# Performance work log

Measured on AMD Instinct MI355X. Metric: run time of the kernel, lower is better.

The kernel has to match this reference:

```python
import jax, jax.numpy as jnp
import numpy as np

D_MODEL = 2048
NUM_HEADS = 16
D_HEAD = D_MODEL // NUM_HEADS
ROPE_THETA = 10000.0
MAX_SEQ_LEN = 2048
NEG_INF = -1e30


def _rope_tables(seq_len):
    pos = jnp.arange(seq_len, dtype=jnp.float32)[:, None]          # [s,1]
    i = jnp.arange(0, D_HEAD, 2, dtype=jnp.float32)                 # [d/2]
    freqs = 1.0 / (ROPE_THETA ** (i / D_HEAD))
    angles = pos * freqs                                            # [s, d/2]
    return jnp.cos(angles), jnp.sin(angles)


def _apply_rope(x, cos, sin):
    # x: [b,h,s,d]; interleaved pairs: x1 = even dims, x2 = odd dims
    x1 = x[..., 0::2]
    x2 = x[..., 1::2]
    r1 = x1 * cos - x2 * sin
    r2 = x1 * sin + x2 * cos
    return jnp.stack([r1, r2], axis=-1).reshape(x.shape)


def setup_inputs() -> dict:
    key = jax.random.key(0)
    ks = jax.random.split(key, 5)
    b, s = 2, 2048
    scale = 1.0 / np.sqrt(D_MODEL)  # ~kaiming fan_in scale
    return {
        "x": jax.random.normal(ks[0], (b, s, D_MODEL), jnp.float32),
        "Wq": jax.random.normal(ks[1], (D_MODEL, D_MODEL), jnp.float32) * scale,
        "bq": jnp.zeros((D_MODEL,), jnp.float32),
        "Wk": jax.random.normal(ks[2], (D_MODEL, D_MODEL), jnp.float32) * scale,
        "bk": jnp.zeros((D_MODEL,), jnp.float32),
        "Wv": jax.random.normal(ks[3], (D_MODEL, D_MODEL), jnp.float32) * scale,
        "bv": jnp.zeros((D_MODEL,), jnp.float32),
        "Wo": jax.random.normal(ks[4], (D_MODEL, D_MODEL), jnp.float32) * scale,
        "bo": jnp.zeros((D_MODEL,), jnp.float32),
    }


def reference(x, Wq, bq, Wk, bk, Wv, bv, Wo, bo):
    b, s, _ = x.shape
    # QKV projections (torch Linear: y = x @ W.T + b)
    q = x @ Wq.T + bq
    k = x @ Wk.T + bk
    v = x @ Wv.T + bv
    # split heads: b s (h d) -> b h s d
    def split(t):
        return t.reshape(b, s, NUM_HEADS, D_HEAD).transpose(0, 2, 1, 3)
    q, k, v = split(q), split(k), split(v)
    # RoPE
    cos, sin = _rope_tables(s)
    q = _apply_rope(q, cos, sin)
    k = _apply_rope(k, cos, sin)
    # scaled dot-product attention with causal mask
    scores = jnp.einsum('bhqd,bhkd->bhqk', q, k) / jnp.sqrt(jnp.float32(D_HEAD))
    causal = jnp.tril(jnp.ones((s, s), dtype=bool))
    scores = jnp.where(causal[None, None], scores, NEG_INF)
    attn = jax.nn.softmax(scores, axis=-1)
    out = jnp.einsum('bhqk,bhkd->bhqd', attn, v)
    # merge heads and output projection
    out = out.transpose(0, 2, 1, 3).reshape(b, s, D_MODEL)
    return out @ Wo.T + bo
```

## Files before the change

### kernel.cpp

```cpp
#include <hip/hip_runtime.h>
#include <hip/hip_fp16.h>
#include <math.h>

#define D_MODEL 2048
#define NH 16
#define DH 128
#define SEQ 2048
#define NBH 32

typedef unsigned short u16;
typedef unsigned int u32;
typedef __attribute__((ext_vector_type(8))) short short8;
typedef __attribute__((ext_vector_type(4))) float floatx4;
typedef __attribute__((ext_vector_type(2))) unsigned int uint2v;
typedef __attribute__((ext_vector_type(4))) unsigned int uint4v;
typedef __attribute__((ext_vector_type(4))) unsigned short ushort4v;

__device__ __forceinline__ u16 f2bf(float f) {
  u32 u = __builtin_bit_cast(u32, f);
  return (u16)((u + 0x8000u) >> 16);
}
__device__ __forceinline__ float bf2f(u16 h) {
  return __builtin_bit_cast(float, (u32)h << 16);
}

__device__ __forceinline__ void async_load16(const u16* g, u16* l) {
  __builtin_amdgcn_global_load_lds(
      (const __attribute__((address_space(1))) void*)g,
      (__attribute__((address_space(3))) void*)l, 16, 0, 0);
}

__global__ void cvt_kernel(const float* __restrict__ src, u16* __restrict__ dst,
                           int n) {
  const int i = (blockIdx.x * 256 + threadIdx.x) * 8;
  if (i >= n) return;
  const floatx4 a = *(const floatx4*)(src + i);
  const floatx4 b = *(const floatx4*)(src + i + 4);
  short8 h;
  h[0] = (short)f2bf(a[0]); h[1] = (short)f2bf(a[1]);
  h[2] = (short)f2bf(a[2]); h[3] = (short)f2bf(a[3]);
  h[4] = (short)f2bf(b[0]); h[5] = (short)f2bf(b[1]);
  h[6] = (short)f2bf(b[2]); h[7] = (short)f2bf(b[3]);
  *(short8*)(dst + i) = h;
}

__global__ void cvt4_kernel(const float* __restrict__ x,
                            const float* __restrict__ wq,
                            const float* __restrict__ wk,
                            const float* __restrict__ wv, u16* __restrict__ xb,
                            u16* __restrict__ wqb, u16* __restrict__ wkb,
                            u16* __restrict__ wvb, u32* __restrict__ rtab) {
  const int blk = blockIdx.x;
  if (blk >= 10240) {
    const int e0 = ((blk - 10240) * 256 + threadIdx.x) * 4;
#pragma unroll
    for (int e = e0; e < e0 + 4; ++e) {
      const int s = e >> 6, p = e & 63;
      const float freq = exp2f(-(float)p * (13.287712379549449f / 64.0f));
      float sn, cs;
      sincosf((float)s * freq, &sn, &cs);
      rtab[e] = (u32)__half_as_ushort(__float2half_rn(cs)) |
                ((u32)__half_as_ushort(__float2half_rn(sn)) << 16);
    }
    return;
  }
  const float* src;
  u16* dst;
  int base;
  if (blk < 4096) {
    src = x; dst = xb; base = blk;
  } else if (blk < 6144) {
    src = wq; dst = wqb; base = blk - 4096;
  } else if (blk < 8192) {
    src = wk; dst = wkb; base = blk - 6144;
  } else {
    src = wv; dst = wvb; base = blk - 8192;
  }
  const int i = (base * 256 + threadIdx.x) * 8;
  const floatx4 a = *(const floatx4*)(src + i);
  const floatx4 b = *(const floatx4*)(src + i + 4);
  short8 h;
  h[0] = (short)f2bf(a[0]); h[1] = (short)f2bf(a[1]);
  h[2] = (short)f2bf(a[2]); h[3] = (short)f2bf(a[3]);
  h[4] = (short)f2bf(b[0]); h[5] = (short)f2bf(b[1]);
  h[6] = (short)f2bf(b[2]); h[7] = (short)f2bf(b[3]);
  *(short8*)(dst + i) = h;
}

__global__ __launch_bounds__(256, 2) void gemm_async(
    const u16* __restrict__ A, const u16* __restrict__ W0,
    const u16* __restrict__ W1, const u16* __restrict__ W2,
    const float* __restrict__ b0, const float* __restrict__ b1,
    const float* __restrict__ b2, void* __restrict__ C0, void* __restrict__ C1,
    void* __restrict__ C2, const u32* __restrict__ rtab, const int qkv) {
  __shared__ u16 smem[2 * 128 * 64];
  u16* const As = smem;
  u16* const Bs = smem + 128 * 64;
  const int tid = threadIdx.x;
  const int wave = tid >> 6, lane = tid & 63;
  const int lr = lane & 15, lg = lane >> 4;
  const int m0 = blockIdx.y * 128;
  const int wm = (wave & 1) * 64, wn = (wave >> 1) * 64;

  int n0, mode;
  const u16* W;
  const float* bias;
  void* C;
  if (qkv) {
    const int which = blockIdx.x >> 4;
    n0 = (blockIdx.x & 15) * 128;
    W = which == 0 ? W0 : which == 1 ? W1 : W2;
    bias = which == 0 ? b0 : which == 1 ? b1 : b2;
    C = which == 0 ? C0 : which == 1 ? C1 : C2;
    mode = which;
  } else {
    n0 = blockIdx.x * 128;
    W = W0; bias = b0; C = C0; mode = 3;
  }

  floatx4 acc[4][4];
#pragma unroll
  for (int i = 0; i < 4; ++i)
#pragma unroll
    for (int j = 0; j < 4; ++j) {
      floatx4 z = {0.f, 0.f, 0.f, 0.f};
      acc[i][j] = z;
    }

  for (int kt = 0; kt < D_MODEL; kt += 64) {
#pragma unroll
    for (int p = 0; p < 4; ++p) {
      const int s = p * 256 + tid;
      const int row = s >> 3, c = s & 7;
      const int g = c ^ (row & 7);
      async_load16(A + (size_t)(m0 + row) * D_MODEL + kt + g * 8,
                   &As[(p * 256 + wave * 64) * 8]);
    }
#pragma unroll
    for (int p = 0; p < 4; ++p) {
      const int s = p * 256 + tid;
      const int row = s >> 3, c = s & 7;
      const int g = c ^ (row & 7);
      async_load16(W + (size_t)(n0 + row) * D_MODEL + kt + g * 8,
                   &Bs[(p * 256 + wave * 64) * 8]);
    }
    __syncthreads();

#pragma unroll
    for (int ks = 0; ks < 2; ++ks) {
      short8 af[4], bfr[4];
      const int ch = (ks * 4 + lg) ^ (lr & 7);
#pragma unroll
      for (int i = 0; i < 4; ++i)
        af[i] = *(const short8*)&As[(wm + 16 * i + lr) * 64 + ch * 8];
#pragma unroll
      for (int j = 0; j < 4; ++j)
        bfr[j] = *(const short8*)&Bs[(wn + 16 * j + lr) * 64 + ch * 8];
#pragma unroll
      for (int i = 0; i < 4; ++i)
#pragma unroll
        for (int j = 0; j < 4; ++j)
          acc[i][j] = __builtin_amdgcn_mfma_f32_16x16x32_bf16(af[i], bfr[j],
                                                              acc[i][j], 0, 0, 0);
    }
    __syncthreads();
  }

  float bj[4];
  int ncol[4];
#pragma unroll
  for (int j = 0; j < 4; ++j) {
    ncol[j] = n0 + wn + 16 * j + lr;
    bj[j] = bias[ncol[j]];
  }

  if (mode == 3) {
    float* Cf = (float*)C;
#pragma unroll
    for (int i = 0; i < 4; ++i)
#pragma unroll
      for (int r = 0; r < 4; ++r) {
        const int m = m0 + wm + 16 * i + lg * 4 + r;
#pragma unroll
        for (int j = 0; j < 4; ++j)
          Cf[(size_t)m * D_MODEL + ncol[j]] = acc[i][j][r] + bj[j];
      }
  } else if (mode == 2) {
    u16* Ch = (u16*)C;
#pragma unroll
    for (int i = 0; i < 4; ++i)
#pragma unroll
      for (int r = 0; r < 4; ++r) {
        const int m = m0 + wm + 16 * i + lg * 4 + r;
        const int b = m >> 11, s = m & (SEQ - 1);
#pragma unroll
        for (int j = 0; j < 4; ++j) {
          const int h = ncol[j] >> 7, d = ncol[j] & (DH - 1);
          Ch[((size_t)((b * NH + h) * DH + d)) * SEQ + s] =
              f2bf(acc[i][j][r] + bj[j]);
        }
      }
  } else {
    u32* tab = (u32*)smem;
    {
      const u32* slice = rtab + (size_t)(m0 & (SEQ - 1)) * 64;
#pragma unroll
      for (int kk = 0; kk < 8; ++kk)
        ((uint4v*)tab)[kk * 256 + tid] = ((const uint4v*)slice)[kk * 256 + tid];
    }
    __syncthreads();
    u16* Ch = (u16*)C;
    int pj[4];
#pragma unroll
    for (int j = 0; j < 4; ++j) pj[j] = (ncol[j] & (DH - 1)) >> 1;
    const bool odd = (lr & 1) != 0;
#pragma unroll
    for (int i = 0; i < 4; ++i)
#pragma unroll
      for (int r = 0; r < 4; ++r) {
        const int mloc = wm + 16 * i + lg * 4 + r;
        const int m = m0 + mloc;
        const int b = m >> 11, s = m & (SEQ - 1);
#pragma unroll
        for (int j = 0; j < 4; ++j) {
          const float val = acc[i][j][r] + bj[j];
          const float partner = __shfl_xor(val, 1);
          const u32 cw = tab[mloc * 64 + pj[j]];
          const float cs = __half2float(__ushort_as_half((u16)(cw & 0xffffu)));
          const float sn = __half2float(__ushort_as_half((u16)(cw >> 16)));
          const float outv = odd ? fmaf(partner, sn, val * cs)
                                 : fmaf(partner, -sn, val * cs);
          const int h = ncol[j] >> 7, d = ncol[j] & (DH - 1);
          Ch[((size_t)((b * NH + h) * SEQ + s)) * DH + d] = f2bf(outv);
        }
      }
  }
}

__global__ void rope_kernel(u16* __restrict__ Q, u16* __restrict__ K) {
  const int idx = blockIdx.x * blockDim.x + threadIdx.x;
  const int p = idx & 63;
  const int s = (idx >> 6) & (SEQ - 1);
  const int bh = idx >> 17;
  if (bh >= NBH) return;
  const float freq = exp2f(-(float)p * (13.287712379549449f / 64.0f));
  const float ang = (float)s * freq;
  float sn, cs;
  sincosf(ang, &sn, &cs);
  const size_t base = ((size_t)bh * SEQ + s) * DH + 2 * p;
  {
    const u32 qq = *(const u32*)(Q + base);
    const float x1 = bf2f((u16)(qq & 0xffffu)), x2 = bf2f((u16)(qq >> 16));
    *(u32*)(Q + base) =
        (u32)f2bf(x1 * cs - x2 * sn) | ((u32)f2bf(x1 * sn + x2 * cs) << 16);
  }
  {
    const u32 kk = *(const u32*)(K + base);
    const float x1 = bf2f((u16)(kk & 0xffffu)), x2 = bf2f((u16)(kk >> 16));
    *(u32*)(K + base) =
        (u32)f2bf(x1 * cs - x2 * sn) | ((u32)f2bf(x1 * sn + x2 * cs) << 16);
  }
}

__global__ __launch_bounds__(256, 2) void attn_kernel(
    const u16* __restrict__ Q, const u16* __restrict__ K,
    const u16* __restrict__ Vt, u16* __restrict__ Oflat) {
  __shared__ u16 Ks[2][64 * 128];
  __shared__ u16 Vts[128 * 64];
  __shared__ u16 Ps[4 * 32 * 72];
  const int tid = threadIdx.x;
  const int wave = tid >> 6, lane = tid & 63;
  const int lr = lane & 15, lg = lane >> 4;
  const int L = blockIdx.y * 16 + blockIdx.x;
  const int bh = L & 31;
  const int t = L >> 5;
  const int qt = (t < 8) ? t : 23 - t;
  const size_t qk0 = (size_t)bh * SEQ * DH;
  const int q0 = qt * 128 + wave * 32;
  const float C = 0.12752602f;
  const float RTHR = 62.7f;

  short8 qf[2][4];
#pragma unroll
  for (int i = 0; i < 2; ++i)
#pragma unroll
    for (int kb = 0; kb < 4; ++kb)
      qf[i][kb] = *(const short8*)(Q + qk0 + (size_t)(q0 + 16 * i + lr) * DH +
                                   kb * 32 + lg * 8);

  floatx4 o[2][9];
#pragma unroll
  for (int i = 0; i < 2; ++i)
#pragma unroll
    for (int jd = 0; jd < 9; ++jd) {
      floatx4 z = {0.f, 0.f, 0.f, 0.f};
      o[i][jd] = z;
    }
  float mrun[2] = {-1e38f, -1e38f};

  const short8 onesv = {16256, 16256, 16256, 16256,
                        16256, 16256, 16256, 16256};

  u16* myP = &Ps[wave * 32 * 72];
  const int nkt = 2 * qt + 2;

#pragma unroll
  for (int p = 0; p < 4; ++p) {
    const int s = p * 256 + tid;
    const int row = s >> 4, c = s & 15;
    const int g = c ^ (row & 15);
    async_load16(K + qk0 + (size_t)row * DH + g * 8,
                 &Ks[0][(p * 256 + wave * 64) * 8]);
  }
  __syncthreads();

  for (int kt = 0; kt < nkt; ++kt) {
    const int cur = kt & 1, nb = cur ^ 1;
    const int kn = (kt + 1 < nkt) ? kt + 1 : kt;
#pragma unroll
    for (int p = 0; p < 4; ++p) {
      const int s = p * 256 + tid;
      const int row = s >> 3, c = s & 7;
      const int g = c ^ (row & 7);
      async_load16(Vt + (size_t)bh * DH * SEQ + (size_t)row * SEQ + kt * 64 + g * 8,
                   &Vts[(p * 256 + wave * 64) * 8]);
    }
#pragma unroll
    for (int p = 0; p < 4; ++p) {
      const int s = p * 256 + tid;
      const int row = s >> 4, c = s & 15;
      const int g = c ^ (row & 15);
      async_load16(K + qk0 + (size_t)(kn * 64 + row) * DH + g * 8,
                   &Ks[nb][(p * 256 + wave * 64) * 8]);
    }

    floatx4 st[4][2];
#pragma unroll
    for (int j = 0; j < 4; ++j)
#pragma unroll
      for (int i = 0; i < 2; ++i) {
        floatx4 z = {0.f, 0.f, 0.f, 0.f};
        st[j][i] = z;
      }
#pragma unroll
    for (int kb = 0; kb < 4; ++kb) {
      short8 kf[4];
#pragma unroll
      for (int j = 0; j < 4; ++j)
        kf[j] = *(const short8*)&Ks[cur][(16 * j + lr) * 128 +
                                         (((kb * 4 + lg) ^ lr)) * 8];
      __builtin_amdgcn_s_setprio(1);
#pragma unroll
      for (int j = 0; j < 4; ++j)
#pragma unroll
        for (int i = 0; i < 2; ++i)
          st[j][i] = __builtin_amdgcn_mfma_f32_16x16x32_bf16(kf[j], qf[i][kb],
                                                             st[j][i], 0, 0, 0);
      __builtin_amdgcn_s_setprio(0);
    }

    if (kt >= 2 * qt) {
#pragma unroll
      for (int j = 0; j < 4; ++j)
#pragma unroll
        for (int i = 0; i < 2; ++i)
#pragma unroll
          for (int r = 0; r < 4; ++r) {
            const int kpos = kt * 64 + 16 * j + 4 * lg + r;
            const int qpos = q0 + 16 * i + lr;
            if (kpos > qpos) st[j][i][r] = -1e30f;
          }
    }

    float mx[2];
#pragma unroll
    for (int i = 0; i < 2; ++i) {
      float m0v = fmaxf(fmaxf(st[0][i][0], st[0][i][1]),
                        fmaxf(st[0][i][2], st[0][i][3]));
      float m1v = fmaxf(fmaxf(st[1][i][0], st[1][i][1]),
                        fmaxf(st[1][i][2], st[1][i][3]));
      float m2v = fmaxf(fmaxf(st[2][i][0], st[2][i][1]),
                        fmaxf(st[2][i][2], st[2][i][3]));
      float m3v = fmaxf(fmaxf(st[3][i][0], st[3][i][1]),
                        fmaxf(st[3][i][2], st[3][i][3]));
      float m = fmaxf(fmaxf(m0v, m1v), fmaxf(m2v, m3v));
      m = fmaxf(m, __shfl_xor(m, 16));
      m = fmaxf(m, __shfl_xor(m, 32));
      mx[i] = m;
    }
    const float grow = fmaxf(mx[0] - mrun[0], mx[1] - mrun[1]);
    if (!__all(grow <= RTHR)) {
      float aS[2];
#pragma unroll
      for (int i = 0; i < 2; ++i) {
        const float mn = fmaxf(mrun[i], mx[i]);
        aS[i] = exp2f((mrun[i] - mn) * C);
        mrun[i] = mn;
      }
#pragma unroll
      for (int i = 0; i < 2; ++i)
#pragma unroll
        for (int r = 0; r < 4; ++r) {
          const float aO = __shfl(aS[i], 4 * lg + r);
#pragma unroll
          for (int jd = 0; jd < 9; ++jd) o[i][jd][r] *= aO;
        }
    }
    float negMC[2];
#pragma unroll
    for (int i = 0; i < 2; ++i) negMC[i] = -mrun[i] * C;

#pragma unroll
    for (int i = 0; i < 2; ++i)
#pragma unroll
      for (int j = 0; j < 4; ++j) {
        const float p0 = exp2f(fmaf(st[j][i][0], C, negMC[i]));
        const float p1 = exp2f(fmaf(st[j][i][1], C, negMC[i]));
        const float p2 = exp2f(fmaf(st[j][i][2], C, negMC[i]));
        const float p3 = exp2f(fmaf(st[j][i][3], C, negMC[i]));
        uint2v w;
        w[0] = (u32)f2bf(p0) | ((u32)f2bf(p1) << 16);
        w[1] = (u32)f2bf(p2) | ((u32)f2bf(p3) << 16);
        *(uint2v*)&myP[(16 * i + lr) * 72 + 16 * j + 4 * lg] = w;
      }

    asm volatile("s_waitcnt lgkmcnt(0)" ::: "memory");
    __syncthreads();

#pragma unroll
    for (int kb = 0; kb < 2; ++kb) {
      short8 pf[2];
#pragma unroll
      for (int i = 0; i < 2; ++i)
        pf[i] = *(const short8*)&myP[(16 * i + lr) * 72 + kb * 32 + lg * 8];
      __builtin_amdgcn_s_setprio(1);
#pragma unroll
      for (int jd = 0; jd < 8; ++jd) {
        const short8 vf = *(const short8*)&Vts[(16 * jd + lr) * 64 +
                                               (((kb * 4 + lg) ^ (lr & 7))) * 8];
#pragma unroll
        for (int i = 0; i < 2; ++i)
          o[i][jd] = __builtin_amdgcn_mfma_f32_16x16x32_bf16(pf[i], vf, o[i][jd],
                                                             0, 0, 0);
      }
#pragma unroll
      for (int i = 0; i < 2; ++i)
        o[i][8] = __builtin_amdgcn_mfma_f32_16x16x32_bf16(pf[i], onesv, o[i][8],
                                                          0, 0, 0);
      __builtin_amdgcn_s_setprio(0);
    }
    __syncthreads();
  }

  const int b = bh >> 4, h = bh & (NH - 1);
#pragma unroll
  for (int i = 0; i < 2; ++i)
#pragma unroll
    for (int r = 0; r < 4; ++r) {
      const int qpos = q0 + 16 * i + lg * 4 + r;
      const float inv = 1.0f / o[i][8][r];
      u16* dst = Oflat + ((size_t)(b * SEQ + qpos)) * D_MODEL + h * DH;
#pragma unroll
      for (int jd = 0; jd < 8; ++jd) dst[16 * jd + lr] = f2bf(o[i][jd][r] * inv);
    }
}

template <int ABF16>
__global__ __launch_bounds__(256, 2) void gemm_kernel(
    const void* __restrict__ Aptr, const float* __restrict__ W,
    const float* __restrict__ bias, void* __restrict__ Cptr, const int mode) {
  __shared__ u16 As[128 * 72];
  __shared__ u16 Bs[128 * 72];
  const int tid = threadIdx.x;
  const int wave = tid >> 6, lane = tid & 63;
  const int lr = lane & 15, lg = lane >> 4;
  const int m0 = blockIdx.y * 128, n0 = blockIdx.x * 128;
  const int wm = (wave & 1) * 64, wn = (wave >> 1) * 64;

  floatx4 acc[4][4];
#pragma unroll
  for (int i = 0; i < 4; ++i)
#pragma unroll
    for (int j = 0; j < 4; ++j) {
      floatx4 z = {0.f, 0.f, 0.f, 0.f};
      acc[i][j] = z;
    }

  for (int kt = 0; kt < D_MODEL; kt += 64) {
    if (ABF16) {
      const u16* A = (const u16*)Aptr;
      const int row0 = tid >> 3, c8 = (tid & 7) * 8;
#pragma unroll
      for (int p = 0; p < 4; ++p) {
        const int row = row0 + p * 32;
        *(short8*)&As[row * 72 + c8] =
            *(const short8*)(A + (size_t)(m0 + row) * D_MODEL + kt + c8);
      }
    } else {
      const float* A = (const float*)Aptr;
      const int row0 = tid >> 4, c4 = (tid & 15) * 4;
#pragma unroll
      for (int p = 0; p < 8; ++p) {
        const int row = row0 + p * 16;
        const floatx4 v =
            *(const floatx4*)(A + (size_t)(m0 + row) * D_MODEL + kt + c4);
        ushort4v h;
        h[0] = f2bf(v[0]); h[1] = f2bf(v[1]); h[2] = f2bf(v[2]); h[3] = f2bf(v[3]);
        *(ushort4v*)&As[row * 72 + c4] = h;
      }
    }
    {
      const int row0 = tid >> 4, c4 = (tid & 15) * 4;
#pragma unroll
      for (int p = 0; p < 8; ++p) {
        const int row = row0 + p * 16;
        const floatx4 v =
            *(const floatx4*)(W + (size_t)(n0 + row) * D_MODEL + kt + c4);
        ushort4v h;
        h[0] = f2bf(v[0]); h[1] = f2bf(v[1]); h[2] = f2bf(v[2]); h[3] = f2bf(v[3]);
        *(ushort4v*)&Bs[row * 72 + c4] = h;
      }
    }
    __syncthreads();
#pragma unroll
    for (int ks = 0; ks < 2; ++ks) {
      short8 af[4], bfr[4];
#pragma unroll
      for (int i = 0; i < 4; ++i)
        af[i] = *(const short8*)&As[(wm + 16 * i + lr) * 72 + ks * 32 + lg * 8];
#pragma unroll
      for (int j = 0; j < 4; ++j)
        bfr[j] = *(const short8*)&Bs[(wn + 16 * j + lr) * 72 + ks * 32 + lg * 8];
#pragma unroll
      for (int i = 0; i < 4; ++i)
#pragma unroll
        for (int j = 0; j < 4; ++j)
          acc[i][j] = __builtin_amdgcn_mfma_f32_16x16x32_bf16(af[i], bfr[j],
                                                              acc[i][j], 0, 0, 0);
    }
    __syncthreads();
  }

  float bj[4];
  int ncol[4];
#pragma unroll
  for (int j = 0; j < 4; ++j) {
    ncol[j] = n0 + wn + 16 * j + lr;
    bj[j] = bias[ncol[j]];
  }

  if (mode == 3) {
    float* C = (float*)Cptr;
#pragma unroll
    for (int i = 0; i < 4; ++i)
#pragma unroll
      for (int r = 0; r < 4; ++r) {
        const int m = m0 + wm + 16 * i + lg * 4 + r;
#pragma unroll
        for (int j = 0; j < 4; ++j)
          C[(size_t)m * D_MODEL + ncol[j]] = acc[i][j][r] + bj[j];
      }
  } else if (mode == 2) {
    u16* C = (u16*)Cptr;
#pragma unroll
    for (int i = 0; i < 4; ++i)
#pragma unroll
      for (int r = 0; r < 4; ++r) {
        const int m = m0 + wm + 16 * i + lg * 4 + r;
        const int b = m >> 11, s = m & (SEQ - 1);
#pragma unroll
        for (int j = 0; j < 4; ++j) {
          const int h = ncol[j] >> 7, d = ncol[j] & (DH - 1);
          C[((size_t)((b * NH + h) * DH + d)) * SEQ + s] = f2bf(acc[i][j][r] + bj[j]);
        }
      }
  } else {
    u16* C = (u16*)Cptr;
#pragma unroll
    for (int i = 0; i < 4; ++i)
#pragma unroll
      for (int r = 0; r < 4; ++r) {
        const int m = m0 + wm + 16 * i + lg * 4 + r;
        const int b = m >> 11, s = m & (SEQ - 1);
#pragma unroll
        for (int j = 0; j < 4; ++j) {
          const int h = ncol[j] >> 7, d = ncol[j] & (DH - 1);
          C[((size_t)((b * NH + h) * SEQ + s)) * DH + d] = f2bf(acc[i][j][r] + bj[j]);
        }
      }
  }
}

extern "C" void kernel_launch(void* const* d_in, const int* in_sizes, int n_in,
                              void* d_out, int out_size, void* d_ws,
                              size_t ws_size, hipStream_t stream) {
  const float* x = (const float*)d_in[0];
  const float* Wq = (const float*)d_in[1];
  const float* bq = (const float*)d_in[2];
  const float* Wk = (const float*)d_in[3];
  const float* bk = (const float*)d_in[4];
  const float* Wv = (const float*)d_in[5];
  const float* bv = (const float*)d_in[6];
  const float* Wo = (const float*)d_in[7];
  const float* bo = (const float*)d_in[8];
  float* out = (float*)d_out;

  const size_t E = (size_t)NBH * SEQ * DH;
  const size_t WE = (size_t)D_MODEL * D_MODEL;
  const size_t need = (4 * E + 3 * WE) * sizeof(u16);

  const dim3 gb(256);

  if (ws_size >= need) {
    u16* xb = (u16*)d_ws;
    u16* wqb = xb + E;
    u16* wkb = wqb + WE;
    u16* wvb = wkb + WE;
    u16* q = wvb + WE;
    u16* k = q + E;
    u16* vt = k + E;
    u16* aflat = xb;
    u16* wob = q;
    u32* rtab = (u32*)out;

    cvt4_kernel<<<dim3(10368), gb, 0, stream>>>(x, Wq, Wk, Wv, xb, wqb, wkb,
                                                wvb, rtab);

    gemm_async<<<dim3(48, 32), gb, 0, stream>>>(xb, wqb, wkb, wvb, bq, bk, bv,
                                                q, k, vt, rtab, 1);
    attn_kernel<<<dim3(SEQ / 128, NBH), gb, 0, stream>>>(q, k, vt, aflat);
    cvt_kernel<<<dim3((int)(WE / 2048)), gb, 0, stream>>>(Wo, wob, (int)WE);
    gemm_async<<<dim3(16, 32), gb, 0, stream>>>(aflat, wob, nullptr, nullptr,
                                                bo, nullptr, nullptr, out,
                                                nullptr, nullptr, nullptr, 0);
  } else {
    u16* q = (u16*)d_ws;
    u16* k = q + E;
    u16* vt = k + E;
    u16* aflat = vt + E;
    const dim3 gg(D_MODEL / 128, (2 * SEQ) / 128);
    gemm_kernel<0><<<gg, gb, 0, stream>>>(x, Wq, bq, q, 0);
    gemm_kernel<0><<<gg, gb, 0, stream>>>(x, Wk, bk, k, 1);
    gemm_kernel<0><<<gg, gb, 0, stream>>>(x, Wv, bv, vt, 2);
    rope_kernel<<<dim3((NBH * SEQ * (DH / 2)) / 256), dim3(256), 0, stream>>>(q, k);
    attn_kernel<<<dim3(SEQ / 128, NBH), gb, 0, stream>>>(q, k, vt, aflat);
    gemm_kernel<1><<<gg, gb, 0, stream>>>(aflat, Wo, bo, out, 3);
  }
}
```

Baseline: 377.5 us.

## Add 256x256-tile QKV GEMM kernel with 512 threads and XCD-aware block remap

Replaces the 128x128-tile QKV projection GEMM with a new kernel that computes 256x256 output tiles using 8 waves and double-buffered async LDS staging. It interleaves the next-tile loads with the MFMA phases and remaps block IDs so neighbouring tiles land on the same XCD. The larger tile raises arithmetic intensity and cuts global and L2 traffic per FLOP. In exchange the grid has only 384 blocks at one block per CU, which risks under-filling the 256 CUs in the last wave, and the fused RoPE/bias epilogue needs a larger register footprint.

```diff
diff --git a/kernel.cpp b/kernel.cpp
--- a/kernel.cpp
+++ b/kernel.cpp
@@ -85,6 +85,173 @@
   h[4] = (short)f2bf(b[0]); h[5] = (short)f2bf(b[1]);
   h[6] = (short)f2bf(b[2]); h[7] = (short)f2bf(b[3]);
   *(short8*)(dst + i) = h;
+}
+
+__global__ __launch_bounds__(512, 1) void gemm256(
+    const u16* __restrict__ A, const u16* __restrict__ W0,
+    const u16* __restrict__ W1, const u16* __restrict__ W2,
+    const float* __restrict__ b0, const float* __restrict__ b1,
+    const float* __restrict__ b2, u16* __restrict__ C0, u16* __restrict__ C1,
+    u16* __restrict__ C2, const u32* __restrict__ rtab) {
+  __shared__ u16 lds[2][2][16384];
+  const int tid = threadIdx.x;
+  const int wid = tid >> 6, lane = tid & 63;
+  const int lr = lane & 15, lg = lane >> 4;
+  const int wm2 = wid >> 2, wn2 = wid & 3;
+
+  const int L = blockIdx.y * 24 + blockIdx.x;
+  const int wg = (L & 7) * 48 + (L >> 3);
+  const int bx = wg % 24, by = wg / 24;
+  const int which = bx >> 3;
+  const int n0 = (bx & 7) * 256;
+  const int m0 = by * 256;
+  const u16* W = which == 0 ? W0 : which == 1 ? W1 : W2;
+  const float* bias = which == 0 ? b0 : which == 1 ? b1 : b2;
+  u16* Ch = which == 0 ? C0 : which == 1 ? C1 : C2;
+
+  auto stage_half = [&](u16* dst, const u16* src, int rowBase, int ktOff) {
+#pragma unroll
+    for (int l = 0; l < 2; ++l) {
+      const int s2 = l * 512 + tid;
+      const int row = s2 >> 3, c = s2 & 7;
+      const int g = c ^ (row & 7);
+      async_load16(src + (size_t)(rowBase + row) * D_MODEL + ktOff + g * 8,
+                   dst + (l * 512 + wid * 64) * 8);
+    }
+  };
+
+  floatx4 acc[8][4];
+#pragma unroll
+  for (int i = 0; i < 8; ++i)
+#pragma unroll
+    for (int j = 0; j < 4; ++j) {
+      floatx4 z = {0.f, 0.f, 0.f, 0.f};
+      acc[i][j] = z;
+    }
+
+  stage_half(&lds[0][0][0],    A, m0,       0);
+  stage_half(&lds[0][0][8192], A, m0 + 128, 0);
+  stage_half(&lds[0][1][0],    W, n0,       0);
+  stage_half(&lds[0][1][8192], W, n0 + 128, 0);
+  __builtin_amdgcn_sched_barrier(0);
+  asm volatile("s_waitcnt vmcnt(0)" ::: "memory");
+  __builtin_amdgcn_sched_barrier(0);
+  __builtin_amdgcn_s_barrier();
+
+  for (int u = 0; u < 32; ++u) {
+    const int cb = u & 1, nb = cb ^ 1;
+    const u16* Ab = &lds[cb][0][0];
+    const u16* Bb = &lds[cb][1][0];
+    u16* An = &lds[nb][0][0];
+    u16* Bn = &lds[nb][1][0];
+    const int kn = (u + 1) * 64;
+    const bool pf = (u + 1 < 32);
+    short8 bfr[4][2];
+#pragma unroll
+    for (int p = 0; p < 4; ++p) {
+      if (p == 0) {
+#pragma unroll
+        for (int j = 0; j < 4; ++j) {
+          const int col = wn2 * 64 + 16 * j + lr;
+#pragma unroll
+          for (int ks = 0; ks < 2; ++ks)
+            bfr[j][ks] =
+                *(const short8*)&Bb[col * 64 + (((ks * 4 + lg) ^ (col & 7))) * 8];
+        }
+      }
+      short8 af[2][2];
+#pragma unroll
+      for (int ii = 0; ii < 2; ++ii) {
+        const int row = wm2 * 128 + 16 * (2 * p + ii) + lr;
+#pragma unroll
+        for (int ks = 0; ks < 2; ++ks)
+          af[ii][ks] =
+              *(const short8*)&Ab[row * 64 + (((ks * 4 + lg) ^ (row & 7))) * 8];
+      }
+      if (pf && p == 0) {
+        stage_half(An,        A, m0,       kn);
+        stage_half(An + 8192, A, m0 + 128, kn);
+      }
+      if (pf && p == 1) {
+        stage_half(Bn,        W, n0,       kn);
+        stage_half(Bn + 8192, W, n0 + 128, kn);
+      }
+      __builtin_amdgcn_sched_barrier(0);
+      __builtin_amdgcn_s_barrier();
+      asm volatile("s_waitcnt lgkmcnt(0)" ::: "memory");
+      __builtin_amdgcn_sched_barrier(0);
+      __builtin_amdgcn_s_setprio(1);
+#pragma unroll
+      for (int ks = 0; ks < 2; ++ks)
+#pragma unroll
+        for (int ii = 0; ii < 2; ++ii)
+#pragma unroll
+          for (int j = 0; j < 4; ++j)
+            acc[2 * p + ii][j] = __builtin_amdgcn_mfma_f32_16x16x32_bf16(
+                af[ii][ks], bfr[j][ks], acc[2 * p + ii][j], 0, 0, 0);
+      __builtin_amdgcn_s_setprio(0);
+      __builtin_amdgcn_sched_barrier(0);
+      if (p == 3 && pf) {
+        asm volatile("s_waitcnt vmcnt(0)" ::: "memory");
+        __builtin_amdgcn_sched_barrier(0);
+      }
+      __builtin_amdgcn_s_barrier();
+    }
+  }
+
+  float bj[4];
+  int ncol[4], pj[4];
+#pragma unroll
+  for (int j = 0; j < 4; ++j) {
+    ncol[j] = n0 + wn2 * 64 + 16 * j + lr;
+    bj[j] = bias[ncol[j]];
+    pj[j] = (ncol[j] & (DH - 1)) >> 1;
+  }
+
+  if (which < 2) {
+    u32* tab = (u32*)&lds[0][0][0];
+    const u32* slice = rtab + (size_t)(m0 & (SEQ - 1)) * 64;
+#pragma unroll
+    for (int kk = 0; kk < 8; ++kk)
+      ((uint4v*)tab)[kk * 512 + tid] = ((const uint4v*)slice)[kk * 512 + tid];
+    __syncthreads();
+    const bool odd = (lr & 1) != 0;
+#pragma unroll
+    for (int i = 0; i < 8; ++i)
+#pragma unroll
+      for (int r = 0; r < 4; ++r) {
+        const int row = wm2 * 128 + 16 * i + 4 * lg + r;
+        const int m = m0 + row;
+        const int b = m >> 11, s = m & (SEQ - 1);
+#pragma unroll
+        for (int j = 0; j < 4; ++j) {
+          const float val = acc[i][j][r] + bj[j];
+          const float partner = __shfl_xor(val, 1);
+          const u32 cw = tab[row * 64 + pj[j]];
+          const float cs = __half2float(__ushort_as_half((u16)(cw & 0xffffu)));
+          const float sn = __half2float(__ushort_as_half((u16)(cw >> 16)));
+          const float outv = odd ? fmaf(partner, sn, val * cs)
+                                 : fmaf(partner, -sn, val * cs);
+          const int h = ncol[j] >> 7, d = ncol[j] & (DH - 1);
+          Ch[((size_t)((b * NH + h) * SEQ + s)) * DH + d] = f2bf(outv);
+        }
+      }
+  } else {
+#pragma unroll
+    for (int i = 0; i < 8; ++i)
+#pragma unroll
+      for (int r = 0; r < 4; ++r) {
+        const int row = wm2 * 128 + 16 * i + 4 * lg + r;
+        const int m = m0 + row;
+        const int b = m >> 11, s = m & (SEQ - 1);
+#pragma unroll
+        for (int j = 0; j < 4; ++j) {
+          const int h = ncol[j] >> 7, d = ncol[j] & (DH - 1);
+          Ch[((size_t)((b * NH + h) * DH + d)) * SEQ + s] =
+              f2bf(acc[i][j][r] + bj[j]);
+        }
+      }
+  }
 }
 
 __global__ __launch_bounds__(256, 2) void gemm_async(
@@ -626,8 +793,8 @@
     cvt4_kernel<<<dim3(10368), gb, 0, stream>>>(x, Wq, Wk, Wv, xb, wqb, wkb,
                                                 wvb, rtab);
 
-    gemm_async<<<dim3(48, 32), gb, 0, stream>>>(xb, wqb, wkb, wvb, bq, bk, bv,
-                                                q, k, vt, rtab, 1);
+    gemm256<<<dim3(24, 16), dim3(512), 0, stream>>>(xb, wqb, wkb, wvb, bq, bk,
+                                                    bv, q, k, vt, rtab);
     attn_kernel<<<dim3(SEQ / 128, NBH), gb, 0, stream>>>(q, k, vt, aflat);
     cvt_kernel<<<dim3((int)(WE / 2048)), gb, 0, stream>>>(Wo, wob, (int)WE);
     gemm_async<<<dim3(16, 32), gb, 0, stream>>>(aflat, wob, nullptr, nullptr,
```

Measured after the change: 383.9 us. About the same (+1.7%).

## Load V fragments directly to registers in attention and fold Wo conversion into cvt4

Applied to the files above, without the earlier changes.

The attention kernel stops staging the transposed V tile through shared memory. Each lane now loads its V MFMA fragments straight from global memory into registers, in two halves placed around the QK^T compute, and one block-wide barrier per iteration is removed. Separately, when the workspace is large enough, the Wo fp32-to-bf16 conversion is merged into the first conversion kernel, which drops one kernel launch. The trade is more register pressure and uncoalesced global reads of V, which rely on L2 reuse, in exchange for less LDS traffic and fewer synchronisations.

```diff
diff --git a/kernel.cpp b/kernel.cpp
--- a/kernel.cpp
+++ b/kernel.cpp
@@ -47,12 +47,14 @@
 __global__ void cvt4_kernel(const float* __restrict__ x,
                             const float* __restrict__ wq,
                             const float* __restrict__ wk,
-                            const float* __restrict__ wv, u16* __restrict__ xb,
+                            const float* __restrict__ wv,
+                            const float* __restrict__ w3, u16* __restrict__ xb,
                             u16* __restrict__ wqb, u16* __restrict__ wkb,
-                            u16* __restrict__ wvb, u32* __restrict__ rtab) {
+                            u16* __restrict__ wvb, u16* __restrict__ w3b,
+                            u32* __restrict__ rtab, const int nconv) {
   const int blk = blockIdx.x;
-  if (blk >= 10240) {
-    const int e0 = ((blk - 10240) * 256 + threadIdx.x) * 4;
+  if (blk >= nconv) {
+    const int e0 = ((blk - nconv) * 256 + threadIdx.x) * 4;
 #pragma unroll
     for (int e = e0; e < e0 + 4; ++e) {
       const int s = e >> 6, p = e & 63;
@@ -73,8 +75,10 @@
     src = wq; dst = wqb; base = blk - 4096;
   } else if (blk < 8192) {
     src = wk; dst = wkb; base = blk - 6144;
+  } else if (blk < 10240) {
+    src = wv; dst = wvb; base = blk - 8192;
   } else {
-    src = wv; dst = wvb; base = blk - 8192;
+    src = w3; dst = w3b; base = blk - 10240;
   }
   const int i = (base * 256 + threadIdx.x) * 8;
   const floatx4 a = *(const floatx4*)(src + i);
@@ -266,7 +270,6 @@
     const u16* __restrict__ Q, const u16* __restrict__ K,
     const u16* __restrict__ Vt, u16* __restrict__ Oflat) {
   __shared__ u16 Ks[2][64 * 128];
-  __shared__ u16 Vts[128 * 64];
   __shared__ u16 Ps[4 * 32 * 72];
   const int tid = threadIdx.x;
   const int wave = tid >> 6, lane = tid & 63;
@@ -303,6 +306,7 @@
 
   u16* myP = &Ps[wave * 32 * 72];
   const int nkt = 2 * qt + 2;
+  const u16* vb = Vt + (size_t)bh * DH * SEQ;
 
 #pragma unroll
   for (int p = 0; p < 4; ++p) {
@@ -317,14 +321,12 @@
   for (int kt = 0; kt < nkt; ++kt) {
     const int cur = kt & 1, nb = cur ^ 1;
     const int kn = (kt + 1 < nkt) ? kt + 1 : kt;
-#pragma unroll
-    for (int p = 0; p < 4; ++p) {
-      const int s = p * 256 + tid;
-      const int row = s >> 3, c = s & 7;
-      const int g = c ^ (row & 7);
-      async_load16(Vt + (size_t)bh * DH * SEQ + (size_t)row * SEQ + kt * 64 + g * 8,
-                   &Vts[(p * 256 + wave * 64) * 8]);
-    }
+
+    short8 v0[8];
+#pragma unroll
+    for (int jd = 0; jd < 8; ++jd)
+      v0[jd] = *(const short8*)(vb + (size_t)(16 * jd + lr) * SEQ + kt * 64 +
+                                lg * 8);
 #pragma unroll
     for (int p = 0; p < 4; ++p) {
       const int s = p * 256 + tid;
@@ -358,6 +360,12 @@
                                                              st[j][i], 0, 0, 0);
       __builtin_amdgcn_s_setprio(0);
     }
+
+    short8 v1[8];
+#pragma unroll
+    for (int jd = 0; jd < 8; ++jd)
+      v1[jd] = *(const short8*)(vb + (size_t)(16 * jd + lr) * SEQ + kt * 64 +
+                                32 + lg * 8);
 
     if (kt >= 2 * qt) {
 #pragma unroll
@@ -425,7 +433,6 @@
       }
 
     asm volatile("s_waitcnt lgkmcnt(0)" ::: "memory");
-    __syncthreads();
 
 #pragma unroll
     for (int kb = 0; kb < 2; ++kb) {
@@ -436,8 +443,7 @@
       __builtin_amdgcn_s_setprio(1);
 #pragma unroll
       for (int jd = 0; jd < 8; ++jd) {
-        const short8 vf = *(const short8*)&Vts[(16 * jd + lr) * 64 +
-                                               (((kb * 4 + lg) ^ (lr & 7))) * 8];
+        const short8 vf = (kb == 0) ? v0[jd] : v1[jd];
 #pragma unroll
         for (int i = 0; i < 2; ++i)
           o[i][jd] = __builtin_amdgcn_mfma_f32_16x16x32_bf16(pf[i], vf, o[i][jd],
@@ -608,6 +614,7 @@
   const size_t E = (size_t)NBH * SEQ * DH;
   const size_t WE = (size_t)D_MODEL * D_MODEL;
   const size_t need = (4 * E + 3 * WE) * sizeof(u16);
+  const size_t need2 = (4 * E + 4 * WE) * sizeof(u16);
 
   const dim3 gb(256);
 
@@ -620,19 +627,31 @@
     u16* k = q + E;
     u16* vt = k + E;
     u16* aflat = xb;
-    u16* wob = q;
     u32* rtab = (u32*)out;
 
-    cvt4_kernel<<<dim3(10368), gb, 0, stream>>>(x, Wq, Wk, Wv, xb, wqb, wkb,
-                                                wvb, rtab);
-
-    gemm_async<<<dim3(48, 32), gb, 0, stream>>>(xb, wqb, wkb, wvb, bq, bk, bv,
-                                                q, k, vt, rtab, 1);
-    attn_kernel<<<dim3(SEQ / 128, NBH), gb, 0, stream>>>(q, k, vt, aflat);
-    cvt_kernel<<<dim3((int)(WE / 2048)), gb, 0, stream>>>(Wo, wob, (int)WE);
-    gemm_async<<<dim3(16, 32), gb, 0, stream>>>(aflat, wob, nullptr, nullptr,
-                                                bo, nullptr, nullptr, out,
-                                                nullptr, nullptr, nullptr, 0);
+    if (ws_size >= need2) {
+      u16* wob = vt + E;
+      cvt4_kernel<<<dim3(12416), gb, 0, stream>>>(x, Wq, Wk, Wv, Wo, xb, wqb,
+                                                  wkb, wvb, wob, rtab, 12288);
+      gemm_async<<<dim3(48, 32), gb, 0, stream>>>(xb, wqb, wkb, wvb, bq, bk,
+                                                  bv, q, k, vt, rtab, 1);
+      attn_kernel<<<dim3(SEQ / 128, NBH), gb, 0, stream>>>(q, k, vt, aflat);
+      gemm_async<<<dim3(16, 32), gb, 0, stream>>>(aflat, wob, nullptr, nullptr,
+                                                  bo, nullptr, nullptr, out,
+                                                  nullptr, nullptr, nullptr, 0);
+    } else {
+      u16* wob = q;
+      cvt4_kernel<<<dim3(10368), gb, 0, stream>>>(x, Wq, Wk, Wv, nullptr, xb,
+                                                  wqb, wkb, wvb, nullptr, rtab,
+                                                  10240);
+      gemm_async<<<dim3(48, 32), gb, 0, stream>>>(xb, wqb, wkb, wvb, bq, bk,
+                                                  bv, q, k, vt, rtab, 1);
+      attn_kernel<<<dim3(SEQ / 128, NBH), gb, 0, stream>>>(q, k, vt, aflat);
+      cvt_kernel<<<dim3((int)(WE / 2048)), gb, 0, stream>>>(Wo, wob, (int)WE);
+      gemm_async<<<dim3(16, 32), gb, 0, stream>>>(aflat, wob, nullptr, nullptr,
+                                                  bo, nullptr, nullptr, out,
+                                                  nullptr, nullptr, nullptr, 0);
+    }
   } else {
     u16* q = (u16*)d_ws;
     u16* k = q + E;
```

Result: slower. 390.6 us (+3.4%).
